# Performance work log

Measured on AMD Instinct MI355X. Metric: run time of the kernel, lower is better.

The kernel has to match this reference:

```python
import jax, jax.numpy as jnp
import numpy as np

N_NODES = 100000
N_EDGES = 1600000
D_IN = 64
D_OUT = 64


def setup_inputs() -> dict:
    key = jax.random.key(0)
    k1, k2, k3, k4, k5, k6, k7 = jax.random.split(key, 7)
    x = jax.random.normal(k1, (N_NODES, D_IN), dtype=jnp.float32)
    edge_index = jax.random.randint(k2, (2, N_EDGES), 0, N_NODES, dtype=jnp.int64)
    pos_encoding = jax.random.normal(k3, (N_NODES, D_IN), dtype=jnp.float32)
    # GCNConv linear weight (no bias inside lin; bias added post-aggregation)
    W_gcn = jax.random.normal(k4, (D_IN, D_OUT), dtype=jnp.float32) / np.sqrt(D_IN)
    b_gcn = jax.random.normal(k5, (D_OUT,), dtype=jnp.float32) * 0.01
    # positional encoding Linear
    W_pos = jax.random.normal(k6, (D_IN, D_OUT), dtype=jnp.float32) / np.sqrt(D_IN)
    b_pos = jax.random.normal(k7, (D_OUT,), dtype=jnp.float32) * 0.01
    return {"x": x, "edge_index": edge_index, "pos_encoding": pos_encoding,
            "W_gcn": W_gcn, "b_gcn": b_gcn, "W_pos": W_pos, "b_pos": b_pos}


def _gcn_conv(x, edge_index, W, b):
    n = x.shape[0]
    # add self-loops (PyG GCNConv default)
    loop = jnp.arange(n, dtype=edge_index.dtype)
    src = jnp.concatenate([edge_index[0], loop])
    dst = jnp.concatenate([edge_index[1], loop])
    # symmetric normalization: deg over destination with unit edge weights
    deg = jax.ops.segment_sum(jnp.ones_like(src, dtype=x.dtype), dst, num_segments=n)
    dinv = jnp.where(deg > 0, jax.lax.rsqrt(deg), 0.0)
    norm = dinv[src] * dinv[dst]  # [E+N]
    h = x @ W  # [N, D_OUT]
    msg = h[src] * norm[:, None]  # gather + scale
    out = jax.ops.segment_sum(msg, dst, num_segments=n)  # scatter-add
    return out + b


def reference(x, edge_index, pos_encoding, W_gcn, b_gcn, W_pos, b_pos):
    conv_out = _gcn_conv(x, edge_index, W_gcn, b_gcn)
    pos = pos_encoding @ W_pos + b_pos
    return conv_out + pos
```

## Files before the change

### kernel.cpp

```cpp
#include <hip/hip_runtime.h>
#include <hip/hip_fp16.h>

#define NN 100000
#define NE 1600000
#define D  64

#define B1     1024
#define BSH    9
#define BMSK   511
#define NB     196
#define STRIDE 16256

typedef __attribute__((ext_vector_type(8))) _Float16 f16x8;
typedef __attribute__((ext_vector_type(4))) float    f32x4;

__global__ __launch_bounds__(256) void k_scatter_fused(
    const int* __restrict__ src, const int* __restrict__ dst,
    int* __restrict__ gcnt, unsigned* __restrict__ ebuf)
{
    __shared__ int h[NB];
    int t = threadIdx.x, blk = blockIdx.x;
    for (int i = t; i < NB; i += 256) h[i] = 0;
    __syncthreads();
    unsigned v[7]; int bn[7]; int cntl = 0;
    int e = blk * 256 + t;
#pragma unroll
    for (int i = 0; i < 7; ++i, e += B1 * 256) {
        if (e < NE) {
            int d = dst[e];
            int s = src[e];
            int b = d >> BSH;
            v[i] = ((unsigned)s << BSH) | (unsigned)(d & BMSK);
            bn[i] = b;
            atomicAdd(&h[b], 1);
            cntl = i + 1;
        }
    }
    __syncthreads();
    for (int i = t; i < NB; i += 256)
        h[i] = atomicAdd(&gcnt[i], h[i]);
    __syncthreads();
#pragma unroll
    for (int i = 0; i < 7; ++i) {
        if (i < cntl) {
            int b = bn[i];
            int p = atomicAdd(&h[b], 1);
            ebuf[b * STRIDE + p] = v[i];
        }
    }
}

__global__ __launch_bounds__(256) void k_scan196(const int* __restrict__ gcnt,
                                                 int* __restrict__ binoff) {
    __shared__ int ps[256];
    int t = threadIdx.x;
    int v = (t < NB) ? gcnt[t] : 0;
    ps[t] = v;
    __syncthreads();
    for (int off = 1; off < 256; off <<= 1) {
        int u = (t >= off) ? ps[t - off] : 0;
        __syncthreads();
        ps[t] += u;
        __syncthreads();
    }
    if (t < NB) binoff[t] = ps[t] - v;
    if (t == NB - 1) binoff[NB] = ps[t];
}

__global__ __launch_bounds__(512) void k_build(
    const int* __restrict__ gcnt, const int* __restrict__ binoff,
    const unsigned* __restrict__ ebuf,
    int* __restrict__ rs, float* __restrict__ dinv, int* __restrict__ bucket)
{
    __shared__ int c[512];
    __shared__ int ps[512];
    int t = threadIdx.x, b = blockIdx.x;
    int e0s = b * STRIDE;
    int cnt = gcnt[b];
    int g0  = binoff[b];
    c[t] = 0;
    __syncthreads();
    for (int e = t; e < cnt; e += 512)
        atomicAdd(&c[ebuf[e0s + e] & BMSK], 1);
    __syncthreads();
    int a = c[t];
    ps[t] = a;
    __syncthreads();
    for (int off = 1; off < 512; off <<= 1) {
        int u = (t >= off) ? ps[t - off] : 0;
        __syncthreads();
        ps[t] += u;
        __syncthreads();
    }
    int p = g0 + ps[t] - a;
    int node = (b << BSH) + t;
    if (node < NN) { rs[node] = p; dinv[node] = rsqrtf((float)(a + 1)); }
    if (b == NB - 1 && t == 0) rs[NN] = NE;
    __syncthreads();
    c[t] = p;
    __syncthreads();
    for (int e = t; e < cnt; e += 512) {
        unsigned u = ebuf[e0s + e];
        int pp = atomicAdd(&c[u & BMSK], 1);
        bucket[pp] = (int)(u >> BSH);
    }
}

__global__ __launch_bounds__(256) void k_mm(
    const float* __restrict__ x, const float* __restrict__ Wg,
    const float* __restrict__ dinv, __half* __restrict__ g,
    const float* __restrict__ pos, const float* __restrict__ Wp,
    const float* __restrict__ bg, const float* __restrict__ bp,
    float* __restrict__ out)
{
    __shared__ __align__(16) _Float16 Wt[64][64];
    int t = threadIdx.x;
    int lane = t & 63;
    int wid = t >> 6;
    int half_grid = gridDim.x >> 1;
    bool job2 = blockIdx.x >= half_grid;
    int blk = job2 ? (blockIdx.x - half_grid) : blockIdx.x;
    const float* A = job2 ? pos : x;
    const float* W = job2 ? Wp : Wg;

    if (blockIdx.x == 0 && t < 64) g[(long)NN * D + t] = __float2half(0.f);

    for (int i = t; i < 64 * 64; i += 256) {
        int k = i >> 6, n = i & 63;
        Wt[n][k] = (_Float16)W[i];
    }
    __syncthreads();

    int lr = lane & 15;
    int lg = lane >> 4;
    int kofs = lg * 8;

    f16x8 b[4][2];
#pragma unroll
    for (int n = 0; n < 4; ++n)
#pragma unroll
        for (int kt = 0; kt < 2; ++kt)
            b[n][kt] = *(const f16x8*)&Wt[n * 16 + lr][kt * 32 + kofs];

    float bsum[4] = {0.f, 0.f, 0.f, 0.f};
    if (job2) {
#pragma unroll
        for (int n = 0; n < 4; ++n) {
            int cc = n * 16 + lr;
            bsum[n] = bg[cc] + bp[cc];
        }
    }

    for (int rb0 = blk * 64; rb0 < NN; rb0 += half_grid * 64) {
        int rb = rb0 + wid * 16;
        int arow = rb + lr;
        int arc = arow < NN ? arow : NN - 1;
        const float4* ap = (const float4*)(A + (long)arc * 64 + kofs);
        float4 p0 = ap[0], p1 = ap[1], p2 = ap[8], p3 = ap[9];
        f16x8 a0, a1;
        a0[0] = (_Float16)p0.x; a0[1] = (_Float16)p0.y;
        a0[2] = (_Float16)p0.z; a0[3] = (_Float16)p0.w;
        a0[4] = (_Float16)p1.x; a0[5] = (_Float16)p1.y;
        a0[6] = (_Float16)p1.z; a0[7] = (_Float16)p1.w;
        a1[0] = (_Float16)p2.x; a1[1] = (_Float16)p2.y;
        a1[2] = (_Float16)p2.z; a1[3] = (_Float16)p2.w;
        a1[4] = (_Float16)p3.x; a1[5] = (_Float16)p3.y;
        a1[6] = (_Float16)p3.z; a1[7] = (_Float16)p3.w;

        f32x4 z = {0.f, 0.f, 0.f, 0.f};
        f32x4 acc[4] = {z, z, z, z};
#pragma unroll
        for (int n = 0; n < 4; ++n) {
            acc[n] = __builtin_amdgcn_mfma_f32_16x16x32_f16(a0, b[n][0], acc[n], 0, 0, 0);
            acc[n] = __builtin_amdgcn_mfma_f32_16x16x32_f16(a1, b[n][1], acc[n], 0, 0, 0);
        }

        int orow0 = rb + lg * 4;
        if (!job2) {
#pragma unroll
            for (int r = 0; r < 4; ++r) {
                int row = orow0 + r;
                if (row < NN) {
                    float di = dinv[row];
#pragma unroll
                    for (int n = 0; n < 4; ++n)
                        g[(long)row * D + n * 16 + lr] = __float2half(acc[n][r] * di);
                }
            }
        } else {
#pragma unroll
            for (int r = 0; r < 4; ++r) {
                int row = orow0 + r;
                if (row < NN) {
#pragma unroll
                    for (int n = 0; n < 4; ++n)
                        out[(long)row * D + n * 16 + lr] = acc[n][r] + bsum[n];
                }
            }
        }
    }
}

__global__ __launch_bounds__(256) void k_gather(
    const int* __restrict__ rs, const int* __restrict__ bucket,
    const float* __restrict__ dinv, const __half* __restrict__ g,
    float* __restrict__ out)
{
    int lane = threadIdx.x & 63;
    int f = lane & 7;
    int grp = lane >> 3;
    int w0 = (blockIdx.x << 2) + (threadIdx.x >> 6);
    int nw = gridDim.x << 2;
    const uint4* gq = (const uint4*)g;

    for (int n0 = w0; n0 < NN; n0 += nw) {
        int node = __builtin_amdgcn_readfirstlane(n0);
        int r0 = rs[node], r1 = rs[node + 1];
        float a0 = 0.f, a1 = 0.f, a2 = 0.f, a3 = 0.f;
        float a4 = 0.f, a5 = 0.f, a6 = 0.f, a7 = 0.f;
        for (int base = r0; base < r1; base += 64) {
            int rem = r1 - base;
            int nl = rem < 64 ? rem : 64;
            int sl = (lane < nl) ? bucket[base + lane] : NN;
            int NG = (nl + 7) >> 3;
#pragma unroll 4
            for (int c = 0; c < NG; ++c) {
                int s = __shfl(sl, c * 8 + grp);
                uint4 u = gq[(long)s * 8 + f];
                __half2 h0 = *(__half2*)&u.x, h1 = *(__half2*)&u.y;
                __half2 h2 = *(__half2*)&u.z, h3 = *(__half2*)&u.w;
                a0 += __low2float(h0); a1 += __high2float(h0);
                a2 += __low2float(h1); a3 += __high2float(h1);
                a4 += __low2float(h2); a5 += __high2float(h2);
                a6 += __low2float(h3); a7 += __high2float(h3);
            }
        }
#pragma unroll
        for (int mask = 8; mask <= 32; mask <<= 1) {
            a0 += __shfl_xor(a0, mask); a1 += __shfl_xor(a1, mask);
            a2 += __shfl_xor(a2, mask); a3 += __shfl_xor(a3, mask);
            a4 += __shfl_xor(a4, mask); a5 += __shfl_xor(a5, mask);
            a6 += __shfl_xor(a6, mask); a7 += __shfl_xor(a7, mask);
        }
        if (lane < 16) {
            int ff = lane & 7, hs = lane >> 3;
            uint4 u = gq[(long)node * 8 + ff];
            __half2 s0 = hs ? *(__half2*)&u.z : *(__half2*)&u.x;
            __half2 s1 = hs ? *(__half2*)&u.w : *(__half2*)&u.y;
            float b0 = hs ? a4 : a0, b1 = hs ? a5 : a1;
            float b2 = hs ? a6 : a2, b3 = hs ? a7 : a3;
            float di = dinv[node];
            float4* op = (float4*)(out + (long)node * D) + (ff * 2 + hs);
            float4 o = *op;
            o.x += (b0 + __low2float(s0)) * di;
            o.y += (b1 + __high2float(s0)) * di;
            o.z += (b2 + __low2float(s1)) * di;
            o.w += (b3 + __high2float(s1)) * di;
            *op = o;
        }
    }
}

extern "C" void kernel_launch(void* const* d_in, const int* in_sizes, int n_in,
                              void* d_out, int out_size, void* d_ws, size_t ws_size,
                              hipStream_t stream) {
    const float* x   = (const float*)d_in[0];
    const int*   ei  = (const int*)d_in[1];
    const float* pos = (const float*)d_in[2];
    const float* Wg  = (const float*)d_in[3];
    const float* bg  = (const float*)d_in[4];
    const float* Wp  = (const float*)d_in[5];
    const float* bp  = (const float*)d_in[6];
    float* out = (float*)d_out;

    const int* src = ei;
    const int* dst = ei + NE;

    char* Wb = (char*)d_ws;
    __half*   g      = (__half*)Wb;
    unsigned* ebuf   = (unsigned*)Wb;
    int*      bucket = (int*)(Wb + 12800256);
    int*      rs     = bucket + NE;
    float*    dinv   = (float*)(rs + NN + 4);
    int*      gcnt   = (int*)(dinv + NN);
    int*      binoff = gcnt + NB;

    hipMemsetAsync(gcnt, 0, NB * sizeof(int), stream);
    hipLaunchKernelGGL(k_scatter_fused, dim3(B1),   dim3(256), 0, stream,
                       src, dst, gcnt, ebuf);
    hipLaunchKernelGGL(k_scan196,       dim3(1),    dim3(256), 0, stream, gcnt, binoff);
    hipLaunchKernelGGL(k_build,         dim3(NB),   dim3(512), 0, stream,
                       gcnt, binoff, ebuf, rs, dinv, bucket);
    hipLaunchKernelGGL(k_mm,            dim3(1564), dim3(256), 0, stream,
                       x, Wg, dinv, g, pos, Wp, bg, bp, out);
    hipLaunchKernelGGL(k_gather,        dim3(2048), dim3(256), 0, stream,
                       rs, bucket, dinv, g, out);
}
```

Measured before the change: 217.5 us.

## Replace binned two-pass CSR build with atomic degree count and multi-block scan

Replaces the bin-based edge bucketing (local histogram, global bin offsets, per-bin local sort) with a direct CSR build: global atomic degree counting, a three-kernel prefix scan, and an atomic-cursor scatter of source indices. The gather kernel now processes four nodes per wavefront, 16 lanes each, instead of one node per wave, which cuts the cross-lane reduction and the idle lanes on low-degree nodes. The new build relies on heavily contended global atomics and random scatter writes and adds launches, which may cost more than the locality the binned approach provided.

```diff
diff --git a/kernel.cpp b/kernel.cpp
--- a/kernel.cpp
+++ b/kernel.cpp
@@ -5,104 +5,78 @@
 #define NE 1600000
 #define D  64
 
-#define B1     1024
-#define BSH    9
-#define BMSK   511
-#define NB     196
-#define STRIDE 16256
+#define SCAN_BLKS 98
 
 typedef __attribute__((ext_vector_type(8))) _Float16 f16x8;
 typedef __attribute__((ext_vector_type(4))) float    f32x4;
 
-__global__ __launch_bounds__(256) void k_scatter_fused(
-    const int* __restrict__ src, const int* __restrict__ dst,
-    int* __restrict__ gcnt, unsigned* __restrict__ ebuf)
-{
-    __shared__ int h[NB];
-    int t = threadIdx.x, blk = blockIdx.x;
-    for (int i = t; i < NB; i += 256) h[i] = 0;
-    __syncthreads();
-    unsigned v[7]; int bn[7]; int cntl = 0;
-    int e = blk * 256 + t;
-#pragma unroll
-    for (int i = 0; i < 7; ++i, e += B1 * 256) {
-        if (e < NE) {
-            int d = dst[e];
-            int s = src[e];
-            int b = d >> BSH;
-            v[i] = ((unsigned)s << BSH) | (unsigned)(d & BMSK);
-            bn[i] = b;
-            atomicAdd(&h[b], 1);
-            cntl = i + 1;
-        }
-    }
-    __syncthreads();
-    for (int i = t; i < NB; i += 256)
-        h[i] = atomicAdd(&gcnt[i], h[i]);
-    __syncthreads();
-#pragma unroll
-    for (int i = 0; i < 7; ++i) {
-        if (i < cntl) {
-            int b = bn[i];
-            int p = atomicAdd(&h[b], 1);
-            ebuf[b * STRIDE + p] = v[i];
-        }
-    }
-}
-
-__global__ __launch_bounds__(256) void k_scan196(const int* __restrict__ gcnt,
-                                                 int* __restrict__ binoff) {
-    __shared__ int ps[256];
-    int t = threadIdx.x;
-    int v = (t < NB) ? gcnt[t] : 0;
+__global__ __launch_bounds__(256) void k_deg(const int* __restrict__ dst,
+                                             int* __restrict__ deg) {
+    for (int e = blockIdx.x * 256 + threadIdx.x; e < NE; e += 1024 * 256)
+        atomicAdd(&deg[dst[e]], 1);
+}
+
+__global__ __launch_bounds__(1024) void k_scanA(const int* __restrict__ deg,
+                                                int* __restrict__ ex,
+                                                int* __restrict__ bsum) {
+    __shared__ int ps[1024];
+    int t = threadIdx.x, b = blockIdx.x;
+    int i = b * 1024 + t;
+    int v = (i < NN) ? deg[i] : 0;
     ps[t] = v;
     __syncthreads();
-    for (int off = 1; off < 256; off <<= 1) {
+    for (int off = 1; off < 1024; off <<= 1) {
         int u = (t >= off) ? ps[t - off] : 0;
         __syncthreads();
         ps[t] += u;
         __syncthreads();
     }
-    if (t < NB) binoff[t] = ps[t] - v;
-    if (t == NB - 1) binoff[NB] = ps[t];
-}
-
-__global__ __launch_bounds__(512) void k_build(
-    const int* __restrict__ gcnt, const int* __restrict__ binoff,
-    const unsigned* __restrict__ ebuf,
-    int* __restrict__ rs, float* __restrict__ dinv, int* __restrict__ bucket)
-{
-    __shared__ int c[512];
-    __shared__ int ps[512];
-    int t = threadIdx.x, b = blockIdx.x;
-    int e0s = b * STRIDE;
-    int cnt = gcnt[b];
-    int g0  = binoff[b];
-    c[t] = 0;
+    if (i < NN) ex[i] = ps[t] - v;
+    if (t == 1023) bsum[b] = ps[t];
+}
+
+__global__ __launch_bounds__(128) void k_scanB(const int* __restrict__ bsum,
+                                               int* __restrict__ boff) {
+    __shared__ int ps[128];
+    int t = threadIdx.x;
+    int v = (t < SCAN_BLKS) ? bsum[t] : 0;
+    ps[t] = v;
     __syncthreads();
-    for (int e = t; e < cnt; e += 512)
-        atomicAdd(&c[ebuf[e0s + e] & BMSK], 1);
-    __syncthreads();
-    int a = c[t];
-    ps[t] = a;
-    __syncthreads();
-    for (int off = 1; off < 512; off <<= 1) {
+    for (int off = 1; off < 128; off <<= 1) {
         int u = (t >= off) ? ps[t - off] : 0;
         __syncthreads();
         ps[t] += u;
         __syncthreads();
     }
-    int p = g0 + ps[t] - a;
-    int node = (b << BSH) + t;
-    if (node < NN) { rs[node] = p; dinv[node] = rsqrtf((float)(a + 1)); }
-    if (b == NB - 1 && t == 0) rs[NN] = NE;
-    __syncthreads();
-    c[t] = p;
-    __syncthreads();
-    for (int e = t; e < cnt; e += 512) {
-        unsigned u = ebuf[e0s + e];
-        int pp = atomicAdd(&c[u & BMSK], 1);
-        bucket[pp] = (int)(u >> BSH);
+    if (t < SCAN_BLKS) boff[t] = ps[t] - v;
+}
+
+__global__ __launch_bounds__(1024) void k_scanC(const int* __restrict__ deg,
+                                                const int* __restrict__ ex,
+                                                const int* __restrict__ boff,
+                                                int* __restrict__ rs,
+                                                int* __restrict__ cur,
+                                                float* __restrict__ dinv) {
+    int b = blockIdx.x;
+    int i = b * 1024 + threadIdx.x;
+    if (i < NN) {
+        int r = ex[i] + boff[b];
+        rs[i] = r;
+        cur[i] = r;
+        int d = deg[i];
+        dinv[i] = rsqrtf((float)(d + 1));
+        if (i == NN - 1) rs[NN] = r + d;
+    }
+}
+
+__global__ __launch_bounds__(256) void k_scatter(const int* __restrict__ src,
+                                                 const int* __restrict__ dst,
+                                                 int* __restrict__ cur,
+                                                 int* __restrict__ bucket) {
+    for (int e = blockIdx.x * 256 + threadIdx.x; e < NE; e += 1024 * 256) {
+        int d = dst[e];
+        int p = atomicAdd(&cur[d], 1);
+        bucket[p] = src[e];
     }
 }
 
@@ -207,25 +181,29 @@
     float* __restrict__ out)
 {
     int lane = threadIdx.x & 63;
-    int f = lane & 7;
-    int grp = lane >> 3;
-    int w0 = (blockIdx.x << 2) + (threadIdx.x >> 6);
-    int nw = gridDim.x << 2;
+    int l    = lane & 15;
+    int f    = l & 7;
+    int hs   = l >> 3;
+    int gb   = lane & 48;
+    int wv   = (blockIdx.x << 2) + (threadIdx.x >> 6);
+    int nw   = gridDim.x << 2;
     const uint4* gq = (const uint4*)g;
 
-    for (int n0 = w0; n0 < NN; n0 += nw) {
-        int node = __builtin_amdgcn_readfirstlane(n0);
+    for (int n0 = (wv << 2); n0 < NN; n0 += (nw << 2)) {
+        int node = n0 + (lane >> 4);
         int r0 = rs[node], r1 = rs[node + 1];
+        int cnt = r1 - r0;
+        int maxc = cnt;
+        maxc = max(maxc, __shfl_xor(maxc, 16));
+        maxc = max(maxc, __shfl_xor(maxc, 32));
         float a0 = 0.f, a1 = 0.f, a2 = 0.f, a3 = 0.f;
         float a4 = 0.f, a5 = 0.f, a6 = 0.f, a7 = 0.f;
-        for (int base = r0; base < r1; base += 64) {
-            int rem = r1 - base;
-            int nl = rem < 64 ? rem : 64;
-            int sl = (lane < nl) ? bucket[base + lane] : NN;
-            int NG = (nl + 7) >> 3;
+        for (int base = 0; base < maxc; base += 16) {
+            int sl = (base + l < cnt) ? bucket[r0 + base + l] : NN;
+            int lim = maxc - base; if (lim > 16) lim = 16;
 #pragma unroll 4
-            for (int c = 0; c < NG; ++c) {
-                int s = __shfl(sl, c * 8 + grp);
+            for (int c2 = 0; c2 < lim; c2 += 2) {
+                int s = __shfl(sl, gb + c2 + hs);
                 uint4 u = gq[(long)s * 8 + f];
                 __half2 h0 = *(__half2*)&u.x, h1 = *(__half2*)&u.y;
                 __half2 h2 = *(__half2*)&u.z, h3 = *(__half2*)&u.w;
@@ -235,29 +213,23 @@
                 a6 += __low2float(h3); a7 += __high2float(h3);
             }
         }
-#pragma unroll
-        for (int mask = 8; mask <= 32; mask <<= 1) {
-            a0 += __shfl_xor(a0, mask); a1 += __shfl_xor(a1, mask);
-            a2 += __shfl_xor(a2, mask); a3 += __shfl_xor(a3, mask);
-            a4 += __shfl_xor(a4, mask); a5 += __shfl_xor(a5, mask);
-            a6 += __shfl_xor(a6, mask); a7 += __shfl_xor(a7, mask);
-        }
-        if (lane < 16) {
-            int ff = lane & 7, hs = lane >> 3;
-            uint4 u = gq[(long)node * 8 + ff];
-            __half2 s0 = hs ? *(__half2*)&u.z : *(__half2*)&u.x;
-            __half2 s1 = hs ? *(__half2*)&u.w : *(__half2*)&u.y;
-            float b0 = hs ? a4 : a0, b1 = hs ? a5 : a1;
-            float b2 = hs ? a6 : a2, b3 = hs ? a7 : a3;
-            float di = dinv[node];
-            float4* op = (float4*)(out + (long)node * D) + (ff * 2 + hs);
-            float4 o = *op;
-            o.x += (b0 + __low2float(s0)) * di;
-            o.y += (b1 + __high2float(s0)) * di;
-            o.z += (b2 + __low2float(s1)) * di;
-            o.w += (b3 + __high2float(s1)) * di;
-            *op = o;
-        }
+        a0 += __shfl_xor(a0, 8); a1 += __shfl_xor(a1, 8);
+        a2 += __shfl_xor(a2, 8); a3 += __shfl_xor(a3, 8);
+        a4 += __shfl_xor(a4, 8); a5 += __shfl_xor(a5, 8);
+        a6 += __shfl_xor(a6, 8); a7 += __shfl_xor(a7, 8);
+        float di = dinv[node];
+        uint4 u = gq[(long)node * 8 + f];
+        __half2 s0 = hs ? *(__half2*)&u.z : *(__half2*)&u.x;
+        __half2 s1 = hs ? *(__half2*)&u.w : *(__half2*)&u.y;
+        float b0 = hs ? a4 : a0, b1 = hs ? a5 : a1;
+        float b2 = hs ? a6 : a2, b3 = hs ? a7 : a3;
+        float4* op = (float4*)(out + (long)node * D) + (f * 2 + hs);
+        float4 o = *op;
+        o.x += (b0 + __low2float(s0)) * di;
+        o.y += (b1 + __high2float(s0)) * di;
+        o.z += (b2 + __low2float(s1)) * di;
+        o.w += (b3 + __high2float(s1)) * di;
+        *op = o;
     }
 }
 
@@ -278,21 +250,25 @@
 
     char* Wb = (char*)d_ws;
     __half*   g      = (__half*)Wb;
-    unsigned* ebuf   = (unsigned*)Wb;
     int*      bucket = (int*)(Wb + 12800256);
-    int*      rs     = bucket + NE;
-    float*    dinv   = (float*)(rs + NN + 4);
-    int*      gcnt   = (int*)(dinv + NN);
-    int*      binoff = gcnt + NB;
-
-    hipMemsetAsync(gcnt, 0, NB * sizeof(int), stream);
-    hipLaunchKernelGGL(k_scatter_fused, dim3(B1),   dim3(256), 0, stream,
-                       src, dst, gcnt, ebuf);
-    hipLaunchKernelGGL(k_scan196,       dim3(1),    dim3(256), 0, stream, gcnt, binoff);
-    hipLaunchKernelGGL(k_build,         dim3(NB),   dim3(512), 0, stream,
-                       gcnt, binoff, ebuf, rs, dinv, bucket);
-    hipLaunchKernelGGL(k_mm,            dim3(1564), dim3(256), 0, stream,
+    int*      deg    = bucket + NE;
+    int*      ex     = deg + NN;
+    int*      rs     = ex + NN;
+    int*      cur    = rs + NN + 4;
+    float*    dinv   = (float*)(cur + NN);
+    int*      bsum   = (int*)(dinv + NN);
+    int*      boff   = bsum + 128;
+
+    hipMemsetAsync(deg, 0, NN * sizeof(int), stream);
+    hipLaunchKernelGGL(k_deg,     dim3(1024),      dim3(256),  0, stream, dst, deg);
+    hipLaunchKernelGGL(k_scanA,   dim3(SCAN_BLKS), dim3(1024), 0, stream, deg, ex, bsum);
+    hipLaunchKernelGGL(k_scanB,   dim3(1),         dim3(128),  0, stream, bsum, boff);
+    hipLaunchKernelGGL(k_scanC,   dim3(SCAN_BLKS), dim3(1024), 0, stream,
+                       deg, ex, boff, rs, cur, dinv);
+    hipLaunchKernelGGL(k_scatter, dim3(1024),      dim3(256),  0, stream,
+                       src, dst, cur, bucket);
+    hipLaunchKernelGGL(k_mm,      dim3(1564),      dim3(256),  0, stream,
                        x, Wg, dinv, g, pos, Wp, bg, bp, out);
-    hipLaunchKernelGGL(k_gather,        dim3(2048), dim3(256), 0, stream,
+    hipLaunchKernelGGL(k_gather,  dim3(2048),      dim3(256),  0, stream,
                        rs, bucket, dinv, g, out);
 }
```

New measurement: 357.6 us. +64.4%, slower.
